# Optimization experiments

Hardware: AMD Instinct MI355X
Metric: run time of the kernel (lower is better)

The kernel has to match this reference:

```python
import jax, jax.numpy as jnp
import numpy as np

N = 50000    # nodes
E = 800000   # edges
F = 128      # node_feature_dim
H = 128      # GCN hidden
H2 = 64      # fc1 hidden
T = 8        # num_tactics
G = 64       # graphs in batch


def setup_inputs() -> dict:
    key = jax.random.key(0)
    ks = jax.random.split(key, 12)
    s = 0.05
    return {
        "x": jax.random.normal(ks[0], (N, F), jnp.float32),
        "edge_index": jax.random.randint(ks[1], (2, E), 0, N, dtype=jnp.int32),
        "batch": jnp.sort(jax.random.randint(ks[2], (N,), 0, G, dtype=jnp.int32)),
        "W": jax.random.normal(ks[3], (F, H), jnp.float32) * s,
        "b": jax.random.normal(ks[4], (H,), jnp.float32) * s,
        "fc1_w": jax.random.normal(ks[5], (H, H2), jnp.float32) * s,
        "fc1_b": jax.random.normal(ks[6], (H2,), jnp.float32) * s,
        "actor_w": jax.random.normal(ks[7], (H2, T), jnp.float32) * s,
        "actor_b": jax.random.normal(ks[8], (T,), jnp.float32) * s,
        "critic_w": jax.random.normal(ks[9], (H2, 1), jnp.float32) * s,
        "critic_b": jax.random.normal(ks[10], (1,), jnp.float32) * s,
    }


def _gcn_conv(x, edge_index, W, b):
    # PyG GCNConv: add self-loops, symmetric D^-1/2 (A+I) D^-1/2 normalization,
    # linear transform first, then scatter-add aggregation, then bias.
    n = x.shape[0]
    loops = jnp.arange(n, dtype=edge_index.dtype)
    src = jnp.concatenate([edge_index[0], loops])  # message sources (x_j)
    dst = jnp.concatenate([edge_index[1], loops])  # aggregation targets
    deg = jax.ops.segment_sum(jnp.ones_like(dst, jnp.float32), dst, num_segments=N)
    dinv = deg ** -0.5  # deg >= 1 due to self-loops
    norm = dinv[src] * dinv[dst]                   # [E+N]
    h = x @ W                                      # [N, H]
    msgs = h[src] * norm[:, None]                  # [E+N, H]
    return jax.ops.segment_sum(msgs, dst, num_segments=N) + b


def reference(x, edge_index, batch, W, b, fc1_w, fc1_b, actor_w, actor_b, critic_w, critic_b):
    h = jax.nn.relu(_gcn_conv(x, edge_index, W, b))            # [N, H]
    # global_mean_pool over batch index
    sums = jax.ops.segment_sum(h, batch, num_segments=G)       # [G, H]
    cnts = jax.ops.segment_sum(jnp.ones((h.shape[0],), h.dtype), batch, num_segments=G)
    group_state = sums / jnp.maximum(cnts, 1.0)[:, None]
    z = jax.nn.relu(group_state @ fc1_w + fc1_b)               # [G, H2]
    tactic_probs = jax.nn.softmax(z @ actor_w + actor_b, axis=-1)  # [G, T]
    group_value = z @ critic_w + critic_b                      # [G, 1]
    return tactic_probs, group_value
```

## Files before the change

### kernel.cpp

```cpp
#include <hip/hip_runtime.h>
#include <hip/hip_bf16.h>

#define NN 50000
#define EE 800000
#define FF 128
#define HH 128
#define HID2 64
#define TT 8
#define GG 64
#define NB 196
#define NSB 256
#define EPB (EE / NSB)
#define NPAD 50048

using frag_ab = __attribute__((ext_vector_type(8))) short;
using frag_cd = __attribute__((ext_vector_type(4))) float;

__device__ inline unsigned short f2bf(float f) {
    union { float f; unsigned u; } v; v.f = f;
    unsigned r = v.u + 0x7fff + ((v.u >> 16) & 1);
    return (unsigned short)(r >> 16);
}

__global__ __launch_bounds__(256) void kconv(const float* __restrict__ x,
                                             unsigned short* __restrict__ x_bf) {
    size_t gid = (size_t)blockIdx.x * 256 + threadIdx.x;
    size_t i8 = gid * 8;
    unsigned short o[8];
    if (i8 < (size_t)NN * 128) {
        const float4* p = (const float4*)(x + i8);
        float4 a = p[0], b = p[1];
        o[0] = f2bf(a.x); o[1] = f2bf(a.y); o[2] = f2bf(a.z); o[3] = f2bf(a.w);
        o[4] = f2bf(b.x); o[5] = f2bf(b.y); o[6] = f2bf(b.z); o[7] = f2bf(b.w);
    } else {
#pragma unroll
        for (int j = 0; j < 8; j++) o[j] = 0;
    }
    *(uint4*)(x_bf + i8) = *(const uint4*)o;
}

__global__ __launch_bounds__(256) void kwt(const float* __restrict__ W,
                                           unsigned short* __restrict__ wt_bf) {
    int gid = blockIdx.x * 256 + threadIdx.x;
    int c = gid >> 7, k = gid & 127;
    wt_bf[gid] = f2bf(W[k * 128 + c]);
}

__global__ __launch_bounds__(256) void kb1(const int* __restrict__ dst,
                                           int* __restrict__ table) {
    __shared__ int cnt[NB];
    int t = threadIdx.x, blk = blockIdx.x;
    for (int i = t; i < NB; i += 256) cnt[i] = 0;
    __syncthreads();
    int e0 = blk * EPB;
    for (int e = e0 + t; e < e0 + EPB; e += 256)
        atomicAdd(&cnt[dst[e] >> 8], 1);
    __syncthreads();
    for (int i = t; i < NB; i += 256) table[blk * NB + i] = cnt[i];
}

__global__ __launch_bounds__(256) void kb2a(int* __restrict__ table,
                                            int* __restrict__ ctot) {
    __shared__ int s[256];
    int t = threadIdx.x, b = blockIdx.x;
    int v = table[t * NB + b];
    s[t] = v;
    __syncthreads();
    for (int off = 1; off < 256; off <<= 1) {
        int a = s[t];
        int w = (t >= off) ? s[t - off] : 0;
        __syncthreads();
        s[t] = a + w;
        __syncthreads();
    }
    table[t * NB + b] = s[t] - v;
    if (t == 255) ctot[b] = s[255];
}

__global__ __launch_bounds__(256) void kb2b(const int* __restrict__ ctot,
                                            int* __restrict__ bbase) {
    __shared__ int s[256];
    int b = threadIdx.x;
    int v = (b < NB) ? ctot[b] : 0;
    s[b] = v;
    __syncthreads();
    for (int off = 1; off < 256; off <<= 1) {
        int a = s[b];
        int w = (b >= off) ? s[b - off] : 0;
        __syncthreads();
        s[b] = a + w;
        __syncthreads();
    }
    if (b < NB) bbase[b] = s[b] - v;
    if (b == 0) bbase[NB] = EE;
}

__global__ __launch_bounds__(256) void kb3(const int* __restrict__ src,
                                           const int* __restrict__ dst,
                                           const int* __restrict__ table,
                                           const int* __restrict__ bbase,
                                           unsigned* __restrict__ etmp) {
    __shared__ int ofs[NB];
    __shared__ int cur[NB];
    int t = threadIdx.x, blk = blockIdx.x;
    for (int i = t; i < NB; i += 256) {
        ofs[i] = table[blk * NB + i] + bbase[i];
        cur[i] = 0;
    }
    __syncthreads();
    int e0 = blk * EPB;
    for (int e = e0 + t; e < e0 + EPB; e += 256) {
        int d = dst[e];
        int b = d >> 8;
        int r = atomicAdd(&cur[b], 1);
        etmp[ofs[b] + r] = ((unsigned)d << 16) | (unsigned)src[e];
    }
}

__global__ __launch_bounds__(256) void k_csr(const unsigned* __restrict__ etmp,
                                             const int* __restrict__ bbase,
                                             int* __restrict__ row_ptr,
                                             float* __restrict__ dinv,
                                             int* __restrict__ srcs) {
    __shared__ int s[256];
    __shared__ int cur[256];
    int t = threadIdx.x, b = blockIdx.x;
    s[t] = 0;
    __syncthreads();
    int e0 = bbase[b], e1 = bbase[b + 1];
    for (int e = e0 + t; e < e1; e += 256)
        atomicAdd(&s[(etmp[e] >> 16) & 255], 1);
    __syncthreads();
    int v = s[t];
    for (int off = 1; off < 256; off <<= 1) {
        int a = s[t];
        int w = (t >= off) ? s[t - off] : 0;
        __syncthreads();
        s[t] = a + w;
        __syncthreads();
    }
    int excl = s[t] - v + e0;
    int node = b * 256 + t;
    if (node < NN) {
        row_ptr[node] = excl;
        dinv[node] = rsqrtf((float)(v + 1));
    }
    if (b == NB - 1 && t == 0) row_ptr[NN] = EE;
    cur[t] = excl;
    __syncthreads();
    for (int e = e0 + t; e < e1; e += 256) {
        unsigned u = etmp[e];
        int slot = atomicAdd(&cur[(u >> 16) & 255], 1);
        srcs[slot] = (int)(u & 0xffffu);
    }
}

__global__ __launch_bounds__(256) void k_gemm(const unsigned short* __restrict__ x_bf,
                                              const unsigned short* __restrict__ wt_bf,
                                              const float* __restrict__ dinv,
                                              unsigned short* __restrict__ hs) {
    int tid = threadIdx.x;
    int w = tid >> 6, lane = tid & 63;
    int m = lane & 15, quad = lane >> 4;
    int r0 = blockIdx.x * 64 + w * 16;
    frag_cd acc[8];
#pragma unroll
    for (int nt = 0; nt < 8; nt++) acc[nt] = frag_cd{0.f, 0.f, 0.f, 0.f};

#pragma unroll
    for (int k0 = 0; k0 < 128; k0 += 32) {
        frag_ab a = *(const frag_ab*)(x_bf + (size_t)(r0 + m) * 128 + k0 + quad * 8);
#pragma unroll
        for (int nt = 0; nt < 8; nt++) {
            frag_ab bfr = *(const frag_ab*)(wt_bf + (size_t)(nt * 16 + m) * 128 + k0 + quad * 8);
            acc[nt] = __builtin_amdgcn_mfma_f32_16x16x32_bf16(a, bfr, acc[nt], 0, 0, 0);
        }
    }
#pragma unroll
    for (int reg = 0; reg < 4; reg++) {
        int gr = r0 + quad * 4 + reg;
        if (gr < NN) {
            float di = dinv[gr];
#pragma unroll
            for (int nt = 0; nt < 8; nt++)
                hs[(size_t)gr * 128 + nt * 16 + m] = f2bf(acc[nt][reg] * di);
        }
    }
}

__global__ __launch_bounds__(256) void k_aggr(const uint4* __restrict__ hs4,
                                              const int* __restrict__ row_ptr,
                                              const int* __restrict__ srcs,
                                              const float* __restrict__ dinv,
                                              const float* __restrict__ bias,
                                              const int* __restrict__ batch,
                                              float* __restrict__ gsum) {
    __shared__ float gacc[8 * 128];
    int tid = threadIdx.x;
    int qid = tid >> 4, sub = tid & 15;
    int i_base = blockIdx.x * 32;
    int g_first = batch[i_base];
    int last = i_base + 31; if (last >= NN) last = NN - 1;
    int gspan = batch[last] - g_first + 1;
    bool lds_pool = (gspan <= 8);
    int slots = lds_pool ? gspan : 0;
    for (int idx = tid; idx < slots * 128; idx += 256) gacc[idx] = 0.f;
    __syncthreads();

    const float4* b4 = (const float4*)(bias + sub * 8);
    float4 bb0 = b4[0], bb1 = b4[1];

    float racc[8];
#pragma unroll
    for (int j = 0; j < 8; j++) racc[j] = 0.f;
    int cur_lg = -1;

    for (int n = 0; n < 2; n++) {
        int i = i_base + qid * 2 + n;
        if (i >= NN) break;
        int lg = batch[i] - g_first;
        if (lg != cur_lg) {
            if (cur_lg >= 0) {
                float* gp = lds_pool ? &gacc[cur_lg * 128 + sub * 8]
                                     : &gsum[(g_first + cur_lg) * 128 + sub * 8];
#pragma unroll
                for (int j = 0; j < 8; j++) atomicAdd(&gp[j], racc[j]);
#pragma unroll
                for (int j = 0; j < 8; j++) racc[j] = 0.f;
            }
            cur_lg = lg;
        }
        float di = dinv[i];
        uint4 su = hs4[(size_t)i * 16 + sub];
        float a0 = __uint_as_float(su.x << 16);
        float a1 = __uint_as_float(su.x & 0xffff0000u);
        float a2 = __uint_as_float(su.y << 16);
        float a3 = __uint_as_float(su.y & 0xffff0000u);
        float a4 = __uint_as_float(su.z << 16);
        float a5 = __uint_as_float(su.z & 0xffff0000u);
        float a6 = __uint_as_float(su.w << 16);
        float a7 = __uint_as_float(su.w & 0xffff0000u);
        int e = row_ptr[i], e1 = row_ptr[i + 1];
        for (; e + 3 < e1; e += 4) {
            int s0 = srcs[e], s1 = srcs[e + 1], s2 = srcs[e + 2], s3 = srcs[e + 3];
            uint4 u0 = hs4[(size_t)s0 * 16 + sub];
            uint4 u1 = hs4[(size_t)s1 * 16 + sub];
            uint4 u2 = hs4[(size_t)s2 * 16 + sub];
            uint4 u3 = hs4[(size_t)s3 * 16 + sub];
            a0 += __uint_as_float(u0.x << 16); a1 += __uint_as_float(u0.x & 0xffff0000u);
            a2 += __uint_as_float(u0.y << 16); a3 += __uint_as_float(u0.y & 0xffff0000u);
            a4 += __uint_as_float(u0.z << 16); a5 += __uint_as_float(u0.z & 0xffff0000u);
            a6 += __uint_as_float(u0.w << 16); a7 += __uint_as_float(u0.w & 0xffff0000u);
            a0 += __uint_as_float(u1.x << 16); a1 += __uint_as_float(u1.x & 0xffff0000u);
            a2 += __uint_as_float(u1.y << 16); a3 += __uint_as_float(u1.y & 0xffff0000u);
            a4 += __uint_as_float(u1.z << 16); a5 += __uint_as_float(u1.z & 0xffff0000u);
            a6 += __uint_as_float(u1.w << 16); a7 += __uint_as_float(u1.w & 0xffff0000u);
            a0 += __uint_as_float(u2.x << 16); a1 += __uint_as_float(u2.x & 0xffff0000u);
            a2 += __uint_as_float(u2.y << 16); a3 += __uint_as_float(u2.y & 0xffff0000u);
            a4 += __uint_as_float(u2.z << 16); a5 += __uint_as_float(u2.z & 0xffff0000u);
            a6 += __uint_as_float(u2.w << 16); a7 += __uint_as_float(u2.w & 0xffff0000u);
            a0 += __uint_as_float(u3.x << 16); a1 += __uint_as_float(u3.x & 0xffff0000u);
            a2 += __uint_as_float(u3.y << 16); a3 += __uint_as_float(u3.y & 0xffff0000u);
            a4 += __uint_as_float(u3.z << 16); a5 += __uint_as_float(u3.z & 0xffff0000u);
            a6 += __uint_as_float(u3.w << 16); a7 += __uint_as_float(u3.w & 0xffff0000u);
        }
        for (; e < e1; ++e) {
            uint4 u0 = hs4[(size_t)srcs[e] * 16 + sub];
            a0 += __uint_as_float(u0.x << 16); a1 += __uint_as_float(u0.x & 0xffff0000u);
            a2 += __uint_as_float(u0.y << 16); a3 += __uint_as_float(u0.y & 0xffff0000u);
            a4 += __uint_as_float(u0.z << 16); a5 += __uint_as_float(u0.z & 0xffff0000u);
            a6 += __uint_as_float(u0.w << 16); a7 += __uint_as_float(u0.w & 0xffff0000u);
        }
        racc[0] += fmaxf(fmaf(a0, di, bb0.x), 0.f);
        racc[1] += fmaxf(fmaf(a1, di, bb0.y), 0.f);
        racc[2] += fmaxf(fmaf(a2, di, bb0.z), 0.f);
        racc[3] += fmaxf(fmaf(a3, di, bb0.w), 0.f);
        racc[4] += fmaxf(fmaf(a4, di, bb1.x), 0.f);
        racc[5] += fmaxf(fmaf(a5, di, bb1.y), 0.f);
        racc[6] += fmaxf(fmaf(a6, di, bb1.z), 0.f);
        racc[7] += fmaxf(fmaf(a7, di, bb1.w), 0.f);
    }
    if (cur_lg >= 0) {
        float* gp = lds_pool ? &gacc[cur_lg * 128 + sub * 8]
                             : &gsum[(g_first + cur_lg) * 128 + sub * 8];
#pragma unroll
        for (int j = 0; j < 8; j++) atomicAdd(&gp[j], racc[j]);
    }
    __syncthreads();
    for (int idx = tid; idx < slots * 128; idx += 256) {
        float v = gacc[idx];
        if (v != 0.f)
            atomicAdd(&gsum[(g_first + (idx >> 7)) * 128 + (idx & 127)], v);
    }
}

__device__ inline int lbound(const int* __restrict__ a, int n, int key) {
    int lo = 0, hi = n;
    while (lo < hi) {
        int mid = (lo + hi) >> 1;
        if (a[mid] < key) lo = mid + 1;
        else hi = mid;
    }
    return lo;
}

__global__ __launch_bounds__(64) void k_head(const float* __restrict__ gsum,
                                             const int* __restrict__ batch,
                                             const float* __restrict__ fc1_w,
                                             const float* __restrict__ fc1_b,
                                             const float* __restrict__ actor_w,
                                             const float* __restrict__ actor_b,
                                             const float* __restrict__ critic_w,
                                             const float* __restrict__ critic_b,
                                             float* __restrict__ out) {
    __shared__ float gs[128];
    __shared__ float zs[64];
    __shared__ float ls[8], es[8];
    int g = blockIdx.x, t = threadIdx.x;
    int lo = lbound(batch, NN, g), hi = lbound(batch, NN, g + 1);
    float invc = 1.f / fmaxf((float)(hi - lo), 1.f);
    gs[t] = gsum[g * 128 + t] * invc;
    gs[t + 64] = gsum[g * 128 + 64 + t] * invc;
    __syncthreads();
    float z = fc1_b[t];
    for (int k = 0; k < 128; k++) z = fmaf(gs[k], fc1_w[k * 64 + t], z);
    zs[t] = fmaxf(z, 0.f);
    __syncthreads();
    if (t < 8) {
        float l = actor_b[t];
        for (int k = 0; k < 64; k++) l = fmaf(zs[k], actor_w[k * 8 + t], l);
        ls[t] = l;
    }
    __syncthreads();
    if (t < 8) {
        float m = ls[0];
#pragma unroll
        for (int j = 1; j < 8; j++) m = fmaxf(m, ls[j]);
        es[t] = expf(ls[t] - m);
    }
    __syncthreads();
    if (t < 8) {
        float ssum = 0.f;
#pragma unroll
        for (int j = 0; j < 8; j++) ssum += es[j];
        out[g * 8 + t] = es[t] / ssum;
    }
    if (t == 32) {
        float v = critic_b[0];
        for (int k = 0; k < 64; k++) v = fmaf(zs[k], critic_w[k], v);
        out[GG * TT + g] = v;
    }
}

extern "C" void kernel_launch(void* const* d_in, const int* in_sizes, int n_in,
                              void* d_out, int out_size, void* d_ws, size_t ws_size,
                              hipStream_t stream) {
    const float* x        = (const float*)d_in[0];
    const int*   ei       = (const int*)d_in[1];
    const int*   batch    = (const int*)d_in[2];
    const float* W        = (const float*)d_in[3];
    const float* b        = (const float*)d_in[4];
    const float* fc1_w    = (const float*)d_in[5];
    const float* fc1_b    = (const float*)d_in[6];
    const float* actor_w  = (const float*)d_in[7];
    const float* actor_b  = (const float*)d_in[8];
    const float* critic_w = (const float*)d_in[9];
    const float* critic_b = (const float*)d_in[10];
    float* out = (float*)d_out;

    char* ws = (char*)d_ws;
    size_t off = 0;
    unsigned short* hs    = (unsigned short*)(ws + off); off += (size_t)NN * 128 * 2 + 64;
    unsigned short* x_bf  = (unsigned short*)(ws + off); off += (size_t)NPAD * 128 * 2;
    unsigned short* wt_bf = (unsigned short*)(ws + off); off += (size_t)128 * 128 * 2;
    float* dinv      = (float*)(ws + off);    off += (size_t)NN * 4;
    int*   row_ptr   = (int*)(ws + off);      off += (size_t)(NN + 1) * 4 + 12;
    int*   srcs      = (int*)(ws + off);      off += (size_t)EE * 4;
    unsigned* etmp   = (unsigned*)(ws + off); off += (size_t)EE * 4;
    int*   table     = (int*)(ws + off);      off += (size_t)NSB * NB * 4;
    int*   bbase     = (int*)(ws + off);      off += (size_t)(NB + 1) * 4 + 12;
    int*   ctot      = (int*)(ws + off);      off += (size_t)NB * 4 + 16;
    float* gsum      = (float*)(ws + off);    off += (size_t)GG * HH * 4;

    hipMemsetAsync(gsum, 0, (size_t)GG * HH * 4, stream);

    const int* src = ei;
    const int* dst = ei + EE;

    kconv<<<(NPAD * 128 / 8 + 255) / 256, 256, 0, stream>>>(x, x_bf);
    kwt<<<64, 256, 0, stream>>>(W, wt_bf);
    kb1<<<NSB, 256, 0, stream>>>(dst, table);
    kb2a<<<NB, 256, 0, stream>>>(table, ctot);
    kb2b<<<1, 256, 0, stream>>>(ctot, bbase);
    kb3<<<NSB, 256, 0, stream>>>(src, dst, table, bbase, etmp);
    k_csr<<<NB, 256, 0, stream>>>(etmp, bbase, row_ptr, dinv, srcs);
    k_gemm<<<NPAD / 64, 256, 0, stream>>>(x_bf, wt_bf, dinv, hs);
    k_aggr<<<(NN + 31) / 32, 256, 0, stream>>>((const uint4*)hs, row_ptr, srcs,
                                               dinv, b, batch, gsum);
    k_head<<<GG, 64, 0, stream>>>(gsum, batch, fc1_w, fc1_b, actor_w, actor_b,
                                  critic_w, critic_b, out);
}
```

Baseline: 199.1 us.

## Fuse x bf16 conversion into GEMM and merge prep kernels and memset

Removes the standalone kernel that converts x to bf16. The GEMM now loads fp32 x directly and converts it in registers, which avoids writing and re-reading a bf16 copy of x. The W transpose and the gsum zeroing move into the degree-count kernel, removing two launches and a memset. The aggregation loop is also unrolled to 8 edges so more gathers are in flight. The trade-off is that the GEMM reads twice the bytes for its A operand and uses more registers in the aggregation loop.

```diff
diff --git a/kernel.cpp b/kernel.cpp
--- a/kernel.cpp
+++ b/kernel.cpp
@@ -22,34 +22,22 @@
     return (unsigned short)(r >> 16);
 }
 
-__global__ __launch_bounds__(256) void kconv(const float* __restrict__ x,
-                                             unsigned short* __restrict__ x_bf) {
-    size_t gid = (size_t)blockIdx.x * 256 + threadIdx.x;
-    size_t i8 = gid * 8;
-    unsigned short o[8];
-    if (i8 < (size_t)NN * 128) {
-        const float4* p = (const float4*)(x + i8);
-        float4 a = p[0], b = p[1];
-        o[0] = f2bf(a.x); o[1] = f2bf(a.y); o[2] = f2bf(a.z); o[3] = f2bf(a.w);
-        o[4] = f2bf(b.x); o[5] = f2bf(b.y); o[6] = f2bf(b.z); o[7] = f2bf(b.w);
-    } else {
-#pragma unroll
-        for (int j = 0; j < 8; j++) o[j] = 0;
-    }
-    *(uint4*)(x_bf + i8) = *(const uint4*)o;
-}
-
-__global__ __launch_bounds__(256) void kwt(const float* __restrict__ W,
-                                           unsigned short* __restrict__ wt_bf) {
-    int gid = blockIdx.x * 256 + threadIdx.x;
-    int c = gid >> 7, k = gid & 127;
-    wt_bf[gid] = f2bf(W[k * 128 + c]);
-}
-
-__global__ __launch_bounds__(256) void kb1(const int* __restrict__ dst,
-                                           int* __restrict__ table) {
+__global__ __launch_bounds__(256) void k_front(const int* __restrict__ dst,
+                                               const float* __restrict__ W,
+                                               int* __restrict__ table,
+                                               unsigned short* __restrict__ wt_bf,
+                                               float* __restrict__ gsum) {
     __shared__ int cnt[NB];
     int t = threadIdx.x, blk = blockIdx.x;
+    if (blk < 64) {
+        int gid = blk * 256 + t;
+        int c = gid >> 7, k = gid & 127;
+        wt_bf[gid] = f2bf(W[k * 128 + c]);
+    }
+    if (blk >= 64 && blk < 96) {
+        int gid = (blk - 64) * 256 + t;
+        gsum[gid] = 0.f;
+    }
     for (int i = t; i < NB; i += 256) cnt[i] = 0;
     __syncthreads();
     int e0 = blk * EPB;
@@ -155,7 +143,7 @@
     }
 }
 
-__global__ __launch_bounds__(256) void k_gemm(const unsigned short* __restrict__ x_bf,
+__global__ __launch_bounds__(256) void k_gemm(const float* __restrict__ x,
                                               const unsigned short* __restrict__ wt_bf,
                                               const float* __restrict__ dinv,
                                               unsigned short* __restrict__ hs) {
@@ -163,13 +151,24 @@
     int w = tid >> 6, lane = tid & 63;
     int m = lane & 15, quad = lane >> 4;
     int r0 = blockIdx.x * 64 + w * 16;
+    int row = r0 + m;
     frag_cd acc[8];
 #pragma unroll
     for (int nt = 0; nt < 8; nt++) acc[nt] = frag_cd{0.f, 0.f, 0.f, 0.f};
 
 #pragma unroll
     for (int k0 = 0; k0 < 128; k0 += 32) {
-        frag_ab a = *(const frag_ab*)(x_bf + (size_t)(r0 + m) * 128 + k0 + quad * 8);
+        unsigned short av[8];
+        if (row < NN) {
+            const float4* p = (const float4*)(x + (size_t)row * 128 + k0 + quad * 8);
+            float4 a0 = p[0], a1 = p[1];
+            av[0] = f2bf(a0.x); av[1] = f2bf(a0.y); av[2] = f2bf(a0.z); av[3] = f2bf(a0.w);
+            av[4] = f2bf(a1.x); av[5] = f2bf(a1.y); av[6] = f2bf(a1.z); av[7] = f2bf(a1.w);
+        } else {
+#pragma unroll
+            for (int j = 0; j < 8; j++) av[j] = 0;
+        }
+        frag_ab a = *(const frag_ab*)av;
 #pragma unroll
         for (int nt = 0; nt < 8; nt++) {
             frag_ab bfr = *(const frag_ab*)(wt_bf + (size_t)(nt * 16 + m) * 128 + k0 + quad * 8);
@@ -187,6 +186,12 @@
         }
     }
 }
+
+#define ACC8(u) \
+    a0 += __uint_as_float((u).x << 16); a1 += __uint_as_float((u).x & 0xffff0000u); \
+    a2 += __uint_as_float((u).y << 16); a3 += __uint_as_float((u).y & 0xffff0000u); \
+    a4 += __uint_as_float((u).z << 16); a5 += __uint_as_float((u).z & 0xffff0000u); \
+    a6 += __uint_as_float((u).w << 16); a7 += __uint_as_float((u).w & 0xffff0000u);
 
 __global__ __launch_bounds__(256) void k_aggr(const uint4* __restrict__ hs4,
                                               const int* __restrict__ row_ptr,
@@ -241,35 +246,31 @@
         float a6 = __uint_as_float(su.w << 16);
         float a7 = __uint_as_float(su.w & 0xffff0000u);
         int e = row_ptr[i], e1 = row_ptr[i + 1];
+        for (; e + 7 < e1; e += 8) {
+            int s0 = srcs[e],     s1 = srcs[e + 1], s2 = srcs[e + 2], s3 = srcs[e + 3];
+            int s4 = srcs[e + 4], s5 = srcs[e + 5], s6 = srcs[e + 6], s7 = srcs[e + 7];
+            uint4 u0 = hs4[(size_t)s0 * 16 + sub];
+            uint4 u1 = hs4[(size_t)s1 * 16 + sub];
+            uint4 u2 = hs4[(size_t)s2 * 16 + sub];
+            uint4 u3 = hs4[(size_t)s3 * 16 + sub];
+            uint4 u4 = hs4[(size_t)s4 * 16 + sub];
+            uint4 u5 = hs4[(size_t)s5 * 16 + sub];
+            uint4 u6 = hs4[(size_t)s6 * 16 + sub];
+            uint4 u7 = hs4[(size_t)s7 * 16 + sub];
+            ACC8(u0) ACC8(u1) ACC8(u2) ACC8(u3)
+            ACC8(u4) ACC8(u5) ACC8(u6) ACC8(u7)
+        }
         for (; e + 3 < e1; e += 4) {
             int s0 = srcs[e], s1 = srcs[e + 1], s2 = srcs[e + 2], s3 = srcs[e + 3];
             uint4 u0 = hs4[(size_t)s0 * 16 + sub];
             uint4 u1 = hs4[(size_t)s1 * 16 + sub];
             uint4 u2 = hs4[(size_t)s2 * 16 + sub];
             uint4 u3 = hs4[(size_t)s3 * 16 + sub];
-            a0 += __uint_as_float(u0.x << 16); a1 += __uint_as_float(u0.x & 0xffff0000u);
-            a2 += __uint_as_float(u0.y << 16); a3 += __uint_as_float(u0.y & 0xffff0000u);
-            a4 += __uint_as_float(u0.z << 16); a5 += __uint_as_float(u0.z & 0xffff0000u);
-            a6 += __uint_as_float(u0.w << 16); a7 += __uint_as_float(u0.w & 0xffff0000u);
-            a0 += __uint_as_float(u1.x << 16); a1 += __uint_as_float(u1.x & 0xffff0000u);
-            a2 += __uint_as_float(u1.y << 16); a3 += __uint_as_float(u1.y & 0xffff0000u);
-            a4 += __uint_as_float(u1.z << 16); a5 += __uint_as_float(u1.z & 0xffff0000u);
-            a6 += __uint_as_float(u1.w << 16); a7 += __uint_as_float(u1.w & 0xffff0000u);
-            a0 += __uint_as_float(u2.x << 16); a1 += __uint_as_float(u2.x & 0xffff0000u);
-            a2 += __uint_as_float(u2.y << 16); a3 += __uint_as_float(u2.y & 0xffff0000u);
-            a4 += __uint_as_float(u2.z << 16); a5 += __uint_as_float(u2.z & 0xffff0000u);
-            a6 += __uint_as_float(u2.w << 16); a7 += __uint_as_float(u2.w & 0xffff0000u);
-            a0 += __uint_as_float(u3.x << 16); a1 += __uint_as_float(u3.x & 0xffff0000u);
-            a2 += __uint_as_float(u3.y << 16); a3 += __uint_as_float(u3.y & 0xffff0000u);
-            a4 += __uint_as_float(u3.z << 16); a5 += __uint_as_float(u3.z & 0xffff0000u);
-            a6 += __uint_as_float(u3.w << 16); a7 += __uint_as_float(u3.w & 0xffff0000u);
+            ACC8(u0) ACC8(u1) ACC8(u2) ACC8(u3)
         }
         for (; e < e1; ++e) {
             uint4 u0 = hs4[(size_t)srcs[e] * 16 + sub];
-            a0 += __uint_as_float(u0.x << 16); a1 += __uint_as_float(u0.x & 0xffff0000u);
-            a2 += __uint_as_float(u0.y << 16); a3 += __uint_as_float(u0.y & 0xffff0000u);
-            a4 += __uint_as_float(u0.z << 16); a5 += __uint_as_float(u0.z & 0xffff0000u);
-            a6 += __uint_as_float(u0.w << 16); a7 += __uint_as_float(u0.w & 0xffff0000u);
+            ACC8(u0)
         }
         racc[0] += fmaxf(fmaf(a0, di, bb0.x), 0.f);
         racc[1] += fmaxf(fmaf(a1, di, bb0.y), 0.f);
@@ -371,7 +372,6 @@
     char* ws = (char*)d_ws;
     size_t off = 0;
     unsigned short* hs    = (unsigned short*)(ws + off); off += (size_t)NN * 128 * 2 + 64;
-    unsigned short* x_bf  = (unsigned short*)(ws + off); off += (size_t)NPAD * 128 * 2;
     unsigned short* wt_bf = (unsigned short*)(ws + off); off += (size_t)128 * 128 * 2;
     float* dinv      = (float*)(ws + off);    off += (size_t)NN * 4;
     int*   row_ptr   = (int*)(ws + off);      off += (size_t)(NN + 1) * 4 + 12;
@@ -382,19 +382,15 @@
     int*   ctot      = (int*)(ws + off);      off += (size_t)NB * 4 + 16;
     float* gsum      = (float*)(ws + off);    off += (size_t)GG * HH * 4;
 
-    hipMemsetAsync(gsum, 0, (size_t)GG * HH * 4, stream);
-
     const int* src = ei;
     const int* dst = ei + EE;
 
-    kconv<<<(NPAD * 128 / 8 + 255) / 256, 256, 0, stream>>>(x, x_bf);
-    kwt<<<64, 256, 0, stream>>>(W, wt_bf);
-    kb1<<<NSB, 256, 0, stream>>>(dst, table);
+    k_front<<<NSB, 256, 0, stream>>>(dst, W, table, wt_bf, gsum);
     kb2a<<<NB, 256, 0, stream>>>(table, ctot);
     kb2b<<<1, 256, 0, stream>>>(ctot, bbase);
     kb3<<<NSB, 256, 0, stream>>>(src, dst, table, bbase, etmp);
     k_csr<<<NB, 256, 0, stream>>>(etmp, bbase, row_ptr, dinv, srcs);
-    k_gemm<<<NPAD / 64, 256, 0, stream>>>(x_bf, wt_bf, dinv, hs);
+    k_gemm<<<NPAD / 64, 256, 0, stream>>>(x, wt_bf, dinv, hs);
     k_aggr<<<(NN + 31) / 32, 256, 0, stream>>>((const uint4*)hs, row_ptr, srcs,
                                                dinv, b, batch, gsum);
     k_head<<<GG, 64, 0, stream>>>(gsum, batch, fc1_w, fc1_b, actor_w, actor_b,
```

Measured after the change: 196.0 us. No clear change (-1.5%).
